# Kernel tuning notes

Hardware: AMD Instinct MI355X
Metric: run time of the kernel (lower is better)

Reference implementation:

```python
import jax, jax.numpy as jnp
import numpy as np
import math

B, L, C = 4096, 64, 256   # L == window_size
H = 8                     # num_heads
META_H = 384


def _rel_coords_log(W):
    # coords = meshgrid(arange(1), arange(W)) -> (2, W); first row is zeros
    c0 = jnp.zeros((W,), jnp.float32)
    c1 = jnp.arange(W, dtype=jnp.float32)
    coords = jnp.stack([c0, c1], axis=0)                      # (2, W)
    rel = coords[:, :, None] - coords[:, None, :]             # (2, W, W)
    rel = rel.transpose(1, 2, 0).reshape(-1, 2)               # (W*W, 2)
    return jnp.sign(rel) * jnp.log1p(jnp.abs(rel))


def setup_inputs() -> dict:
    key = jax.random.key(0)
    ks = jax.random.split(key, 8)
    s = 0.02
    return {
        "x": jax.random.normal(ks[0], (B, L, C), jnp.float32),
        "qkv_w": jax.random.normal(ks[1], (3 * C, C), jnp.float32) * s,
        "qkv_b": jnp.zeros((3 * C,), jnp.float32),
        "proj_w": jax.random.normal(ks[2], (C, C), jnp.float32) * s,
        "proj_b": jnp.zeros((C,), jnp.float32),
        "logit_scale": jnp.full((H,), math.log(10.0), jnp.float32),
        "mlp1_w": jax.random.normal(ks[3], (META_H, 2), jnp.float32) * s,
        "mlp1_b": jnp.zeros((META_H,), jnp.float32),
        "mlp2_w": jax.random.normal(ks[4], (H, META_H), jnp.float32) * s,
        "mlp2_b": jnp.zeros((H,), jnp.float32),
    }


def reference(x, qkv_w, qkv_b, proj_w, proj_b, logit_scale, mlp1_w, mlp1_b, mlp2_w, mlp2_b):
    b, l, c = x.shape
    h = H
    d = c // h
    qkv = x @ qkv_w.T + qkv_b                                 # (B, L, 3C)
    qkv = qkv.reshape(b, l, 3, h, d).transpose(2, 0, 3, 1, 4) # (3, B, H, L, D)
    q, k, v = qkv[0], qkv[1], qkv[2]
    # cosine attention: L2-normalize q, k (F.normalize, eps=1e-12)
    qn = q / jnp.maximum(jnp.linalg.norm(q, axis=-1, keepdims=True), 1e-12)
    kn = k / jnp.maximum(jnp.linalg.norm(k, axis=-1, keepdims=True), 1e-12)
    attn = jnp.einsum("bhld,bhmd->bhlm", qn, kn)              # (B, H, L, L)
    scale = jnp.exp(jnp.minimum(logit_scale, math.log(1.0 / 0.01)))
    attn = attn * scale.reshape(1, h, 1, 1)
    # MLP relative position bias
    rel = _rel_coords_log(l)                                  # (L*L, 2)
    hid = jax.nn.relu(rel @ mlp1_w.T + mlp1_b)                # (L*L, META_H)
    bias = (hid @ mlp2_w.T + mlp2_b).T.reshape(h, l, l)       # (H, L, L)
    attn = jax.nn.softmax(attn + bias[None], axis=-1)
    out = jnp.einsum("bhlm,bhmd->bhld", attn, v)              # (B, H, L, D)
    out = out.transpose(0, 2, 1, 3).reshape(b, l, c)
    return out @ proj_w.T + proj_b
```

## Files before the change

### kernel.cpp

```cpp
#include <hip/hip_runtime.h>
#include <hip/hip_bf16.h>

typedef __attribute__((ext_vector_type(4))) float f32x4;
typedef __attribute__((ext_vector_type(8))) short short8;
typedef __attribute__((ext_vector_type(4))) short short4_t;

#define NWIN 4096
#define LTOK 64
#define CDIM 256

static __device__ __forceinline__ short f2bf(float f) {
    __hip_bfloat16 h = __float2bfloat16(f);
    union { __hip_bfloat16 b; short s; } u; u.b = h;
    return u.s;
}

__global__ void prep_weights(const float* __restrict__ qw, const float* __restrict__ pw,
                             short* __restrict__ wqs, short* __restrict__ wps) {
    int i = blockIdx.x * 256 + threadIdx.x;
    if (i < 768 * 256) {
        int row = i >> 8, col = i & 255;
        int nt = row >> 4, lcr = row & 15;
        int kt = col >> 5, lg = (col >> 3) & 3, j = col & 7;
        wqs[(size_t)(((nt * 8 + kt) * 64) + lg * 16 + lcr) * 8 + j] = f2bf(qw[i]);
    }
    if (i < 256 * 256) {
        int row = i >> 8, col = i & 255;
        int ww = row >> 6, ntl = (row >> 4) & 3, lcr = row & 15;
        int h = col >> 5, lg = (col >> 3) & 3, j = col & 7;
        wps[(size_t)((((ww * 4 + ntl) * 8 + h) * 64) + lg * 16 + lcr) * 8 + j] = f2bf(pw[i]);
    }
}

__global__ void prep_bias(const float* __restrict__ w1, const float* __restrict__ b1,
                          const float* __restrict__ w2, const float* __restrict__ b2,
                          const float* __restrict__ lsc, float* __restrict__ biasT,
                          float* __restrict__ scT) {
    int t = threadIdx.x;
    if (t < 8) scT[t] = expf(fminf(lsc[t], logf(100.0f)));
    if (t < 127) {
        float delta = (float)(t - 63);
        float sg = (delta > 0.f) ? 1.f : ((delta < 0.f) ? -1.f : 0.f);
        float r = sg * log1pf(fabsf(delta));
        float acc[8];
        #pragma unroll
        for (int q = 0; q < 8; ++q) acc[q] = b2[q];
        for (int m = 0; m < 384; ++m) {
            float hid = fmaxf(fmaf(r, w1[m * 2 + 1], b1[m]), 0.f);
            #pragma unroll
            for (int q = 0; q < 8; ++q) acc[q] = fmaf(hid, w2[q * 384 + m], acc[q]);
        }
        #pragma unroll
        for (int q = 0; q < 8; ++q) biasT[q * 127 + t] = acc[q];
    }
}


__global__ void __launch_bounds__(256, 2)
fused_win_attn(const float* __restrict__ x,
               const float* __restrict__ qkv_b,
               const float* __restrict__ proj_b,
               const short* __restrict__ wqs,
               const short* __restrict__ wps,
               const float* __restrict__ biasT,
               const float* __restrict__ scT,
               float* __restrict__ out)
{
    __shared__ short XS[64 * 264];
    __shared__ short QG[64 * 72];
    __shared__ short KG[64 * 72];
    __shared__ short VT[64 * 72];
    __shared__ short PB[64 * 72];
    __shared__ short AO[64 * 40];
    __shared__ float NSQ[2 * 64 * 4];

    const int tid = threadIdx.x;
    const int w  = tid >> 6;
    const int l  = tid & 63;
    const int lg = l >> 4;
    const int lc = l & 15;
    const int blk = blockIdx.x;

    {
        const float* xb = x + (size_t)blk * (LTOK * CDIM);
        #pragma unroll
        for (int u = 0; u < 8; ++u) {
            int base = u * 2048 + tid * 8;
            f32x4 a = *(const f32x4*)(xb + base);
            f32x4 b = *(const f32x4*)(xb + base + 4);
            int r = base >> 8;
            int c = base & 255;
            short8 t;
            t[0] = f2bf(a[0]); t[1] = f2bf(a[1]); t[2] = f2bf(a[2]); t[3] = f2bf(a[3]);
            t[4] = f2bf(b[0]); t[5] = f2bf(b[1]); t[6] = f2bf(b[2]); t[7] = f2bf(b[3]);
            *(short8*)(XS + r * 264 + c) = t;
        }
    }

    f32x4 accP[4][4];
    #pragma unroll
    for (int a = 0; a < 4; ++a)
        #pragma unroll
        for (int bb = 0; bb < 4; ++bb)
            accP[a][bb] = (f32x4){0.f, 0.f, 0.f, 0.f};

    const f32x4 fzero = {0.f, 0.f, 0.f, 0.f};
    __syncthreads();

    #pragma unroll 1
    for (int g = 0; g < 4; ++g) {
        #pragma unroll
        for (int s = 0; s < 3; ++s) {
            const int cbt = s * 16 + g * 4 + w;
            const float bq = qkv_b[s * 256 + g * 64 + w * 16 + lc];
            f32x4 acc[4];
            acc[0] = acc[1] = acc[2] = acc[3] = fzero;
            #pragma unroll
            for (int kt = 0; kt < 8; ++kt) {
                short8 Bf = *(const short8*)(wqs + (size_t)((cbt * 8 + kt) * 64 + l) * 8);
                #pragma unroll
                for (int mt = 0; mt < 4; ++mt) {
                    short8 Af = *(const short8*)(XS + (mt * 16 + lc) * 264 + kt * 32 + lg * 8);
                    acc[mt] = __builtin_amdgcn_mfma_f32_16x16x32_bf16(Af, Bf, acc[mt], 0, 0, 0);
                }
            }
            if (s < 2) {
                short* dst = (s == 0) ? QG : KG;
                #pragma unroll
                for (int mt = 0; mt < 4; ++mt) {
                    #pragma unroll
                    for (int i = 0; i < 4; ++i) {
                        float v = acc[mt][i] + bq;
                        dst[(mt * 16 + lg * 4 + i) * 72 + (w * 16 + lc)] = f2bf(v);
                        float t = v * v;
                        t += __shfl_xor(t, 1);
                        t += __shfl_xor(t, 2);
                        t += __shfl_xor(t, 4);
                        t += __shfl_xor(t, 8);
                        if (lc == 0) NSQ[s * 256 + (mt * 16 + lg * 4 + i) * 4 + w] = t;
                    }
                }
            } else {
                #pragma unroll
                for (int mt = 0; mt < 4; ++mt) {
                    short4_t pk;
                    #pragma unroll
                    for (int i = 0; i < 4; ++i) pk[i] = f2bf(acc[mt][i] + bq);
                    *(short4_t*)(VT + (w * 16 + lc) * 72 + mt * 16 + lg * 4) = pk;
                }
            }
        }
        __syncthreads();

        #pragma unroll 1
        for (int hh = 0; hh < 2; ++hh) {
            const int h = 2 * g + hh;
            const float sc = scT[h];
            short8 Aq = *(const short8*)(QG + (w * 16 + lc) * 72 + hh * 32 + lg * 8);
            f32x4 pacc[4];
            #pragma unroll
            for (int nt = 0; nt < 4; ++nt) {
                short8 Bk = *(const short8*)(KG + (nt * 16 + lc) * 72 + hh * 32 + lg * 8);
                pacc[nt] = __builtin_amdgcn_mfma_f32_16x16x32_bf16(Aq, Bk, fzero, 0, 0, 0);
            }
            float invq[4], invk[4];
            #pragma unroll
            for (int i = 0; i < 4; ++i) {
                int r = w * 16 + lg * 4 + i;
                invq[i] = rsqrtf(NSQ[r * 4 + 2 * hh] + NSQ[r * 4 + 2 * hh + 1] + 1e-24f) * sc;
            }
            #pragma unroll
            for (int nt = 0; nt < 4; ++nt) {
                int rk = nt * 16 + lc;
                invk[nt] = rsqrtf(NSQ[256 + rk * 4 + 2 * hh] + NSQ[256 + rk * 4 + 2 * hh + 1] + 1e-24f);
            }
            float p[4][4];
            #pragma unroll
            for (int i = 0; i < 4; ++i) {
                int r = w * 16 + lg * 4 + i;
                #pragma unroll
                for (int nt = 0; nt < 4; ++nt) {
                    int c = nt * 16 + lc;
                    p[i][nt] = pacc[nt][i] * invq[i] * invk[nt] + biasT[h * 127 + r - c + 63];
                }
            }
            #pragma unroll
            for (int i = 0; i < 4; ++i) {
                float m = fmaxf(fmaxf(p[i][0], p[i][1]), fmaxf(p[i][2], p[i][3]));
                m = fmaxf(m, __shfl_xor(m, 1));
                m = fmaxf(m, __shfl_xor(m, 2));
                m = fmaxf(m, __shfl_xor(m, 4));
                m = fmaxf(m, __shfl_xor(m, 8));
                float ssum = 0.f;
                #pragma unroll
                for (int nt = 0; nt < 4; ++nt) { p[i][nt] = __expf(p[i][nt] - m); ssum += p[i][nt]; }
                ssum += __shfl_xor(ssum, 1);
                ssum += __shfl_xor(ssum, 2);
                ssum += __shfl_xor(ssum, 4);
                ssum += __shfl_xor(ssum, 8);
                float rinv = 1.f / ssum;
                #pragma unroll
                for (int nt = 0; nt < 4; ++nt)
                    PB[(w * 16 + lg * 4 + i) * 72 + nt * 16 + lc] = f2bf(p[i][nt] * rinv);
            }
            __syncthreads();

            f32x4 oacc[2];
            oacc[0] = oacc[1] = fzero;
            #pragma unroll
            for (int kt = 0; kt < 2; ++kt) {
                short8 Ap = *(const short8*)(PB + (w * 16 + lc) * 72 + kt * 32 + lg * 8);
                #pragma unroll
                for (int nt2 = 0; nt2 < 2; ++nt2) {
                    short8 Bv = *(const short8*)(VT + (hh * 32 + nt2 * 16 + lc) * 72 + kt * 32 + lg * 8);
                    oacc[nt2] = __builtin_amdgcn_mfma_f32_16x16x32_bf16(Ap, Bv, oacc[nt2], 0, 0, 0);
                }
            }
            #pragma unroll
            for (int nt2 = 0; nt2 < 2; ++nt2)
                #pragma unroll
                for (int i = 0; i < 4; ++i)
                    AO[(w * 16 + lg * 4 + i) * 40 + nt2 * 16 + lc] = f2bf(oacc[nt2][i]);
            __syncthreads();

            #pragma unroll
            for (int mt = 0; mt < 4; ++mt) {
                short8 Aa = *(const short8*)(AO + (mt * 16 + lc) * 40 + lg * 8);
                #pragma unroll
                for (int ntl = 0; ntl < 4; ++ntl) {
                    short8 Bp = *(const short8*)(wps + (size_t)(((w * 4 + ntl) * 8 + h) * 64 + l) * 8);
                    accP[mt][ntl] = __builtin_amdgcn_mfma_f32_16x16x32_bf16(Aa, Bp, accP[mt][ntl], 0, 0, 0);
                }
            }
        }
    }

    {
        float* ob = out + (size_t)blk * (LTOK * CDIM);
        float pbv[4];
        #pragma unroll
        for (int ntl = 0; ntl < 4; ++ntl) pbv[ntl] = proj_b[w * 64 + ntl * 16 + lc];
        #pragma unroll
        for (int mt = 0; mt < 4; ++mt)
            #pragma unroll
            for (int ntl = 0; ntl < 4; ++ntl)
                #pragma unroll
                for (int i = 0; i < 4; ++i)
                    ob[(mt * 16 + lg * 4 + i) * 256 + w * 64 + ntl * 16 + lc] = accP[mt][ntl][i] + pbv[ntl];
    }
}

extern "C" void kernel_launch(void* const* d_in, const int* in_sizes, int n_in,
                              void* d_out, int out_size, void* d_ws, size_t ws_size,
                              hipStream_t stream) {
    const float* x     = (const float*)d_in[0];
    const float* qkvw  = (const float*)d_in[1];
    const float* qkvb  = (const float*)d_in[2];
    const float* projw = (const float*)d_in[3];
    const float* projb = (const float*)d_in[4];
    const float* lsc   = (const float*)d_in[5];
    const float* w1    = (const float*)d_in[6];
    const float* b1    = (const float*)d_in[7];
    const float* w2    = (const float*)d_in[8];
    const float* b2    = (const float*)d_in[9];
    float* out = (float*)d_out;

    short* wqs   = (short*)d_ws;
    short* wps   = (short*)((char*)d_ws + 393216);
    float* biasT = (float*)((char*)d_ws + 524288);
    float* scT   = (float*)((char*)d_ws + 528384);

    const int nwin = in_sizes[0] / (LTOK * CDIM);

    prep_weights<<<768, 256, 0, stream>>>(qkvw, projw, wqs, wps);
    prep_bias<<<1, 128, 0, stream>>>(w1, b1, w2, b2, lsc, biasT, scT);
    fused_win_attn<<<nwin, 256, 0, stream>>>(x, qkvb, projb, wqs, wps, biasT, scT, out);
}
```

Before: 583.8 us.

## Use 512-thread blocks with per-head wave split and streamed x staging

Doubles the block to 8 waves. The QKV projection is split so each wave computes 3 column strips over 2 row tiles, and the two heads of a group run concurrently on wave halves with double PB/AO buffers. The full bf16 copy of x in LDS is replaced by a small fragment-layout buffer refilled from global memory in two K-halves on every head group, so x is re-read from global four times. This shrinks LDS use and raises per-CU wave count, at the cost of extra global traffic and more barriers.

```diff
diff --git a/kernel.cpp b/kernel.cpp
--- a/kernel.cpp
+++ b/kernel.cpp
@@ -5,7 +5,6 @@
 typedef __attribute__((ext_vector_type(8))) short short8;
 typedef __attribute__((ext_vector_type(4))) short short4_t;
 
-#define NWIN 4096
 #define LTOK 64
 #define CDIM 256
 
@@ -26,9 +25,9 @@
     }
     if (i < 256 * 256) {
         int row = i >> 8, col = i & 255;
-        int ww = row >> 6, ntl = (row >> 4) & 3, lcr = row & 15;
+        int gs = row >> 4, lcr = row & 15;
         int h = col >> 5, lg = (col >> 3) & 3, j = col & 7;
-        wps[(size_t)((((ww * 4 + ntl) * 8 + h) * 64) + lg * 16 + lcr) * 8 + j] = f2bf(pw[i]);
+        wps[(size_t)(((gs * 8 + h) * 64) + lg * 16 + lcr) * 8 + j] = f2bf(pw[i]);
     }
 }
 
@@ -56,7 +55,7 @@
 }
 
 
-__global__ void __launch_bounds__(256, 2)
+__global__ void __launch_bounds__(512, 4)
 fused_win_attn(const float* __restrict__ x,
                const float* __restrict__ qkv_b,
                const float* __restrict__ proj_b,
@@ -66,13 +65,13 @@
                const float* __restrict__ scT,
                float* __restrict__ out)
 {
-    __shared__ short XS[64 * 264];
+    __shared__ short XSF[16 * 64 * 8];
     __shared__ short QG[64 * 72];
     __shared__ short KG[64 * 72];
     __shared__ short VT[64 * 72];
-    __shared__ short PB[64 * 72];
-    __shared__ short AO[64 * 40];
-    __shared__ float NSQ[2 * 64 * 4];
+    __shared__ short PBs[2][64 * 72];
+    __shared__ short AOs[2][64 * 40];
+    __shared__ float NSQ[512];
 
     const int tid = threadIdx.x;
     const int w  = tid >> 6;
@@ -81,82 +80,98 @@
     const int lc = l & 15;
     const int blk = blockIdx.x;
 
-    {
-        const float* xb = x + (size_t)blk * (LTOK * CDIM);
-        #pragma unroll
-        for (int u = 0; u < 8; ++u) {
-            int base = u * 2048 + tid * 8;
-            f32x4 a = *(const f32x4*)(xb + base);
-            f32x4 b = *(const f32x4*)(xb + base + 4);
-            int r = base >> 8;
-            int c = base & 255;
-            short8 t;
-            t[0] = f2bf(a[0]); t[1] = f2bf(a[1]); t[2] = f2bf(a[2]); t[3] = f2bf(a[3]);
-            t[4] = f2bf(b[0]); t[5] = f2bf(b[1]); t[6] = f2bf(b[2]); t[7] = f2bf(b[3]);
-            *(short8*)(XS + r * 264 + c) = t;
-        }
-    }
-
-    f32x4 accP[4][4];
+    const float* xb = x + (size_t)blk * (LTOK * CDIM);
+
+    const int sb  = (w & 3) * 3;
+    const int mtb = (w >> 2) * 2;
+    const int hh  = w >> 2;
+    const int mw  = w & 3;
+
+    const int mtA = w & 3,        kA = w >> 2;
+    const int mtB = (8 + w) & 3,  kB = (8 + w) >> 2;
+    const float* gA = xb + (size_t)(mtA * 16 + lc) * CDIM + lg * 8;
+    const float* gB = xb + (size_t)(mtB * 16 + lc) * CDIM + lg * 8;
+    short* sA = XSF + (size_t)(w * 64 + l) * 8;
+    short* sB = XSF + (size_t)((8 + w) * 64 + l) * 8;
+
+    f32x4 accP[4][2];
     #pragma unroll
-    for (int a = 0; a < 4; ++a)
-        #pragma unroll
-        for (int bb = 0; bb < 4; ++bb)
-            accP[a][bb] = (f32x4){0.f, 0.f, 0.f, 0.f};
-
+    for (int a = 0; a < 4; ++a) { accP[a][0] = (f32x4){0,0,0,0}; accP[a][1] = (f32x4){0,0,0,0}; }
     const f32x4 fzero = {0.f, 0.f, 0.f, 0.f};
-    __syncthreads();
 
     #pragma unroll 1
     for (int g = 0; g < 4; ++g) {
-        #pragma unroll
-        for (int s = 0; s < 3; ++s) {
-            const int cbt = s * 16 + g * 4 + w;
-            const float bq = qkv_b[s * 256 + g * 64 + w * 16 + lc];
-            f32x4 acc[4];
-            acc[0] = acc[1] = acc[2] = acc[3] = fzero;
-            #pragma unroll
-            for (int kt = 0; kt < 8; ++kt) {
-                short8 Bf = *(const short8*)(wqs + (size_t)((cbt * 8 + kt) * 64 + l) * 8);
-                #pragma unroll
-                for (int mt = 0; mt < 4; ++mt) {
-                    short8 Af = *(const short8*)(XS + (mt * 16 + lc) * 264 + kt * 32 + lg * 8);
-                    acc[mt] = __builtin_amdgcn_mfma_f32_16x16x32_bf16(Af, Bf, acc[mt], 0, 0, 0);
-                }
-            }
-            if (s < 2) {
-                short* dst = (s == 0) ? QG : KG;
-                #pragma unroll
-                for (int mt = 0; mt < 4; ++mt) {
+        f32x4 acc[3][2];
+        #pragma unroll
+        for (int t = 0; t < 3; ++t) { acc[t][0] = fzero; acc[t][1] = fzero; }
+
+        #pragma unroll 1
+        for (int ht = 0; ht < 2; ++ht) {
+            {
+                f32x4 a0 = *(const f32x4*)(gA + (ht * 4 + kA) * 32);
+                f32x4 a1 = *(const f32x4*)(gA + (ht * 4 + kA) * 32 + 4);
+                f32x4 b0 = *(const f32x4*)(gB + (ht * 4 + kB) * 32);
+                f32x4 b1 = *(const f32x4*)(gB + (ht * 4 + kB) * 32 + 4);
+                short8 ta, tb;
+                ta[0]=f2bf(a0[0]); ta[1]=f2bf(a0[1]); ta[2]=f2bf(a0[2]); ta[3]=f2bf(a0[3]);
+                ta[4]=f2bf(a1[0]); ta[5]=f2bf(a1[1]); ta[6]=f2bf(a1[2]); ta[7]=f2bf(a1[3]);
+                tb[0]=f2bf(b0[0]); tb[1]=f2bf(b0[1]); tb[2]=f2bf(b0[2]); tb[3]=f2bf(b0[3]);
+                tb[4]=f2bf(b1[0]); tb[5]=f2bf(b1[1]); tb[6]=f2bf(b1[2]); tb[7]=f2bf(b1[3]);
+                *(short8*)sA = ta;
+                *(short8*)sB = tb;
+            }
+            __syncthreads();
+            #pragma unroll
+            for (int ktL = 0; ktL < 4; ++ktL) {
+                short8 Af0 = *(const short8*)(XSF + (size_t)((ktL * 4 + mtb) * 64 + l) * 8);
+                short8 Af1 = *(const short8*)(XSF + (size_t)((ktL * 4 + mtb + 1) * 64 + l) * 8);
+                #pragma unroll
+                for (int tt = 0; tt < 3; ++tt) {
+                    const int strip = sb + tt;
+                    const int gnt = (strip >> 2) * 16 + g * 4 + (strip & 3);
+                    short8 Bf = *(const short8*)(wqs + (size_t)((gnt * 8 + ht * 4 + ktL) * 64 + l) * 8);
+                    acc[tt][0] = __builtin_amdgcn_mfma_f32_16x16x32_bf16(Af0, Bf, acc[tt][0], 0, 0, 0);
+                    acc[tt][1] = __builtin_amdgcn_mfma_f32_16x16x32_bf16(Af1, Bf, acc[tt][1], 0, 0, 0);
+                }
+            }
+            __syncthreads();
+        }
+
+        #pragma unroll
+        for (int tt = 0; tt < 3; ++tt) {
+            const int strip = sb + tt;
+            const int s = strip >> 2, nt = strip & 3;
+            const float bq = qkv_b[s * 256 + g * 64 + nt * 16 + lc];
+            #pragma unroll
+            for (int m = 0; m < 2; ++m) {
+                const int mt = mtb + m;
+                if (s == 2) {
+                    short4_t pk;
+                    #pragma unroll
+                    for (int i = 0; i < 4; ++i) pk[i] = f2bf(acc[tt][m][i] + bq);
+                    *(short4_t*)(VT + (nt * 16 + lc) * 72 + mt * 16 + lg * 4) = pk;
+                } else {
+                    short* dst = s ? KG : QG;
                     #pragma unroll
                     for (int i = 0; i < 4; ++i) {
-                        float v = acc[mt][i] + bq;
-                        dst[(mt * 16 + lg * 4 + i) * 72 + (w * 16 + lc)] = f2bf(v);
-                        float t = v * v;
-                        t += __shfl_xor(t, 1);
-                        t += __shfl_xor(t, 2);
-                        t += __shfl_xor(t, 4);
-                        t += __shfl_xor(t, 8);
-                        if (lc == 0) NSQ[s * 256 + (mt * 16 + lg * 4 + i) * 4 + w] = t;
+                        float v = acc[tt][m][i] + bq;
+                        dst[(mt * 16 + lg * 4 + i) * 72 + nt * 16 + lc] = f2bf(v);
+                        float t2 = v * v;
+                        t2 += __shfl_xor(t2, 1);
+                        t2 += __shfl_xor(t2, 2);
+                        t2 += __shfl_xor(t2, 4);
+                        t2 += __shfl_xor(t2, 8);
+                        if (lc == 0) NSQ[s * 256 + (mt * 16 + lg * 4 + i) * 4 + nt] = t2;
                     }
                 }
-            } else {
-                #pragma unroll
-                for (int mt = 0; mt < 4; ++mt) {
-                    short4_t pk;
-                    #pragma unroll
-                    for (int i = 0; i < 4; ++i) pk[i] = f2bf(acc[mt][i] + bq);
-                    *(short4_t*)(VT + (w * 16 + lc) * 72 + mt * 16 + lg * 4) = pk;
-                }
             }
         }
         __syncthreads();
 
-        #pragma unroll 1
-        for (int hh = 0; hh < 2; ++hh) {
+        {
             const int h = 2 * g + hh;
             const float sc = scT[h];
-            short8 Aq = *(const short8*)(QG + (w * 16 + lc) * 72 + hh * 32 + lg * 8);
+            short8 Aq = *(const short8*)(QG + (mw * 16 + lc) * 72 + hh * 32 + lg * 8);
             f32x4 pacc[4];
             #pragma unroll
             for (int nt = 0; nt < 4; ++nt) {
@@ -166,7 +181,7 @@
             float invq[4], invk[4];
             #pragma unroll
             for (int i = 0; i < 4; ++i) {
-                int r = w * 16 + lg * 4 + i;
+                int r = mw * 16 + lg * 4 + i;
                 invq[i] = rsqrtf(NSQ[r * 4 + 2 * hh] + NSQ[r * 4 + 2 * hh + 1] + 1e-24f) * sc;
             }
             #pragma unroll
@@ -177,7 +192,7 @@
             float p[4][4];
             #pragma unroll
             for (int i = 0; i < 4; ++i) {
-                int r = w * 16 + lg * 4 + i;
+                int r = mw * 16 + lg * 4 + i;
                 #pragma unroll
                 for (int nt = 0; nt < 4; ++nt) {
                     int c = nt * 16 + lc;
@@ -201,15 +216,17 @@
                 float rinv = 1.f / ssum;
                 #pragma unroll
                 for (int nt = 0; nt < 4; ++nt)
-                    PB[(w * 16 + lg * 4 + i) * 72 + nt * 16 + lc] = f2bf(p[i][nt] * rinv);
-            }
-            __syncthreads();
-
+                    PBs[hh][(mw * 16 + lg * 4 + i) * 72 + nt * 16 + lc] = f2bf(p[i][nt] * rinv);
+            }
+        }
+        __syncthreads();
+
+        {
             f32x4 oacc[2];
-            oacc[0] = oacc[1] = fzero;
+            oacc[0] = fzero; oacc[1] = fzero;
             #pragma unroll
             for (int kt = 0; kt < 2; ++kt) {
-                short8 Ap = *(const short8*)(PB + (w * 16 + lc) * 72 + kt * 32 + lg * 8);
+                short8 Ap = *(const short8*)(PBs[hh] + (mw * 16 + lc) * 72 + kt * 32 + lg * 8);
                 #pragma unroll
                 for (int nt2 = 0; nt2 < 2; ++nt2) {
                     short8 Bv = *(const short8*)(VT + (hh * 32 + nt2 * 16 + lc) * 72 + kt * 32 + lg * 8);
@@ -220,33 +237,35 @@
             for (int nt2 = 0; nt2 < 2; ++nt2)
                 #pragma unroll
                 for (int i = 0; i < 4; ++i)
-                    AO[(w * 16 + lg * 4 + i) * 40 + nt2 * 16 + lc] = f2bf(oacc[nt2][i]);
-            __syncthreads();
-
+                    AOs[hh][(mw * 16 + lg * 4 + i) * 40 + nt2 * 16 + lc] = f2bf(oacc[nt2][i]);
+        }
+        __syncthreads();
+
+        #pragma unroll
+        for (int hh2 = 0; hh2 < 2; ++hh2) {
+            const int h2 = 2 * g + hh2;
+            short8 Bp0 = *(const short8*)(wps + (size_t)((((w * 2 + 0) * 8 + h2) * 64) + l) * 8);
+            short8 Bp1 = *(const short8*)(wps + (size_t)((((w * 2 + 1) * 8 + h2) * 64) + l) * 8);
             #pragma unroll
             for (int mt = 0; mt < 4; ++mt) {
-                short8 Aa = *(const short8*)(AO + (mt * 16 + lc) * 40 + lg * 8);
-                #pragma unroll
-                for (int ntl = 0; ntl < 4; ++ntl) {
-                    short8 Bp = *(const short8*)(wps + (size_t)(((w * 4 + ntl) * 8 + h) * 64 + l) * 8);
-                    accP[mt][ntl] = __builtin_amdgcn_mfma_f32_16x16x32_bf16(Aa, Bp, accP[mt][ntl], 0, 0, 0);
-                }
+                short8 Aa = *(const short8*)(AOs[hh2] + (mt * 16 + lc) * 40 + lg * 8);
+                accP[mt][0] = __builtin_amdgcn_mfma_f32_16x16x32_bf16(Aa, Bp0, accP[mt][0], 0, 0, 0);
+                accP[mt][1] = __builtin_amdgcn_mfma_f32_16x16x32_bf16(Aa, Bp1, accP[mt][1], 0, 0, 0);
             }
         }
     }
 
     {
         float* ob = out + (size_t)blk * (LTOK * CDIM);
-        float pbv[4];
-        #pragma unroll
-        for (int ntl = 0; ntl < 4; ++ntl) pbv[ntl] = proj_b[w * 64 + ntl * 16 + lc];
+        float pb0 = proj_b[w * 32 + lc];
+        float pb1 = proj_b[w * 32 + 16 + lc];
         #pragma unroll
         for (int mt = 0; mt < 4; ++mt)
             #pragma unroll
-            for (int ntl = 0; ntl < 4; ++ntl)
-                #pragma unroll
-                for (int i = 0; i < 4; ++i)
-                    ob[(mt * 16 + lg * 4 + i) * 256 + w * 64 + ntl * 16 + lc] = accP[mt][ntl][i] + pbv[ntl];
+            for (int i = 0; i < 4; ++i) {
+                ob[(size_t)(mt * 16 + lg * 4 + i) * 256 + w * 32 + lc]      = accP[mt][0][i] + pb0;
+                ob[(size_t)(mt * 16 + lg * 4 + i) * 256 + w * 32 + 16 + lc] = accP[mt][1][i] + pb1;
+            }
     }
 }
 
@@ -274,5 +293,5 @@
 
     prep_weights<<<768, 256, 0, stream>>>(qkvw, projw, wqs, wps);
     prep_bias<<<1, 128, 0, stream>>>(w1, b1, w2, b2, lsc, biasT, scT);
-    fused_win_attn<<<nwin, 256, 0, stream>>>(x, qkvb, projb, wqs, wps, biasT, scT, out);
-}
+    fused_win_attn<<<nwin, 512, 0, stream>>>(x, qkvb, projb, wqs, wps, biasT, scT, out);
+}
```

Result: slower. 786.2 us (+34.7%).

## Keep X in registers, fragment-layout LDS, per-wave P buffer, batched projection

Applied to the files above, without the earlier changes.

Each wave now owns 16 token rows and holds its bf16 X fragments in registers, so the X staging area in LDS and its barrier are gone. Q, K, V, P and attention outputs are stored in a padded MFMA-fragment LDS layout. Each wave keeps its own softmax buffer, which drops the per-head barriers, and q norms are reduced in registers. The output projection runs once per head pair after a single barrier, and the smaller LDS footprint allows three blocks per CU. The risks are higher register pressure from the X fragments and the larger accumulator, which could cause spills under the tighter launch bound.

```diff
diff --git a/kernel.cpp b/kernel.cpp
--- a/kernel.cpp
+++ b/kernel.cpp
@@ -5,15 +5,16 @@
 typedef __attribute__((ext_vector_type(8))) short short8;
 typedef __attribute__((ext_vector_type(4))) short short4_t;
 
-#define NWIN 4096
 #define LTOK 64
 #define CDIM 256
+#define FRS 576
 
 static __device__ __forceinline__ short f2bf(float f) {
     __hip_bfloat16 h = __float2bfloat16(f);
     union { __hip_bfloat16 b; short s; } u; u.b = h;
     return u.s;
 }
+static __device__ __forceinline__ int KL(int l) { return l + (l >> 3); }
 
 __global__ void prep_weights(const float* __restrict__ qw, const float* __restrict__ pw,
                              short* __restrict__ wqs, short* __restrict__ wps) {
@@ -26,9 +27,9 @@
     }
     if (i < 256 * 256) {
         int row = i >> 8, col = i & 255;
-        int ww = row >> 6, ntl = (row >> 4) & 3, lcr = row & 15;
+        int gs = row >> 4, lcr = row & 15;
         int h = col >> 5, lg = (col >> 3) & 3, j = col & 7;
-        wps[(size_t)((((ww * 4 + ntl) * 8 + h) * 64) + lg * 16 + lcr) * 8 + j] = f2bf(pw[i]);
+        wps[(size_t)(((gs * 8 + h) * 64) + lg * 16 + lcr) * 8 + j] = f2bf(pw[i]);
     }
 }
 
@@ -56,7 +57,7 @@
 }
 
 
-__global__ void __launch_bounds__(256, 2)
+__global__ void __launch_bounds__(256, 3)
 fused_win_attn(const float* __restrict__ x,
                const float* __restrict__ qkv_b,
                const float* __restrict__ proj_b,
@@ -66,34 +67,35 @@
                const float* __restrict__ scT,
                float* __restrict__ out)
 {
-    __shared__ short XS[64 * 264];
-    __shared__ short QG[64 * 72];
-    __shared__ short KG[64 * 72];
-    __shared__ short VT[64 * 72];
-    __shared__ short PB[64 * 72];
-    __shared__ short AO[64 * 40];
-    __shared__ float NSQ[2 * 64 * 4];
+    __shared__ short SH[23040];
+    __shared__ float NSQK[128];
 
     const int tid = threadIdx.x;
     const int w  = tid >> 6;
     const int l  = tid & 63;
     const int lg = l >> 4;
     const int lc = l & 15;
+    const int li4 = lg * 4;
     const int blk = blockIdx.x;
-
+    const int klb = KL(l) * 8;
+
+    short* QGF = SH;
+    short* KGF = SH + 4608;
+    short* VTF = SH + 9216;
+    short* AOF = SH + 13824;
+    short* PW  = SH + 18432 + w * (2 * FRS);
+
+    short8 xf[8];
     {
-        const float* xb = x + (size_t)blk * (LTOK * CDIM);
-        #pragma unroll
-        for (int u = 0; u < 8; ++u) {
-            int base = u * 2048 + tid * 8;
-            f32x4 a = *(const f32x4*)(xb + base);
-            f32x4 b = *(const f32x4*)(xb + base + 4);
-            int r = base >> 8;
-            int c = base & 255;
+        const float* xr = x + (size_t)blk * (LTOK * CDIM) + (size_t)(w * 16 + lc) * CDIM + lg * 8;
+        #pragma unroll
+        for (int kt = 0; kt < 8; ++kt) {
+            f32x4 a = *(const f32x4*)(xr + kt * 32);
+            f32x4 b = *(const f32x4*)(xr + kt * 32 + 4);
             short8 t;
-            t[0] = f2bf(a[0]); t[1] = f2bf(a[1]); t[2] = f2bf(a[2]); t[3] = f2bf(a[3]);
-            t[4] = f2bf(b[0]); t[5] = f2bf(b[1]); t[6] = f2bf(b[2]); t[7] = f2bf(b[3]);
-            *(short8*)(XS + r * 264 + c) = t;
+            t[0]=f2bf(a[0]); t[1]=f2bf(a[1]); t[2]=f2bf(a[2]); t[3]=f2bf(a[3]);
+            t[4]=f2bf(b[0]); t[5]=f2bf(b[1]); t[6]=f2bf(b[2]); t[7]=f2bf(b[3]);
+            xf[kt] = t;
         }
     }
 
@@ -101,88 +103,97 @@
     #pragma unroll
     for (int a = 0; a < 4; ++a)
         #pragma unroll
-        for (int bb = 0; bb < 4; ++bb)
-            accP[a][bb] = (f32x4){0.f, 0.f, 0.f, 0.f};
-
+        for (int b = 0; b < 4; ++b) accP[a][b] = (f32x4){0,0,0,0};
     const f32x4 fzero = {0.f, 0.f, 0.f, 0.f};
-    __syncthreads();
 
     #pragma unroll 1
     for (int g = 0; g < 4; ++g) {
-        #pragma unroll
-        for (int s = 0; s < 3; ++s) {
-            const int cbt = s * 16 + g * 4 + w;
-            const float bq = qkv_b[s * 256 + g * 64 + w * 16 + lc];
-            f32x4 acc[4];
-            acc[0] = acc[1] = acc[2] = acc[3] = fzero;
+        float rnq[2][4], rnk[2][4];
+        #pragma unroll
+        for (int hh = 0; hh < 2; ++hh)
+            #pragma unroll
+            for (int i = 0; i < 4; ++i) { rnq[hh][i] = 1e-24f; rnk[hh][i] = 1e-24f; }
+
+        #pragma unroll
+        for (int sg = 0; sg < 6; ++sg) {
+            const int st0 = sg * 2, st1 = sg * 2 + 1;
+            const int gnt0 = (st0 >> 2) * 16 + g * 4 + (st0 & 3);
+            const int gnt1 = (st1 >> 2) * 16 + g * 4 + (st1 & 3);
+            const short* wb0 = wqs + ((size_t)(gnt0 * 8) * 64 + l) * 8;
+            const short* wb1 = wqs + ((size_t)(gnt1 * 8) * 64 + l) * 8;
+            f32x4 a0 = fzero, a1 = fzero;
             #pragma unroll
             for (int kt = 0; kt < 8; ++kt) {
-                short8 Bf = *(const short8*)(wqs + (size_t)((cbt * 8 + kt) * 64 + l) * 8);
-                #pragma unroll
-                for (int mt = 0; mt < 4; ++mt) {
-                    short8 Af = *(const short8*)(XS + (mt * 16 + lc) * 264 + kt * 32 + lg * 8);
-                    acc[mt] = __builtin_amdgcn_mfma_f32_16x16x32_bf16(Af, Bf, acc[mt], 0, 0, 0);
-                }
-            }
-            if (s < 2) {
-                short* dst = (s == 0) ? QG : KG;
-                #pragma unroll
-                for (int mt = 0; mt < 4; ++mt) {
+                short8 Bf0 = *(const short8*)(wb0 + kt * 512);
+                short8 Bf1 = *(const short8*)(wb1 + kt * 512);
+                a0 = __builtin_amdgcn_mfma_f32_16x16x32_bf16(xf[kt], Bf0, a0, 0, 0, 0);
+                a1 = __builtin_amdgcn_mfma_f32_16x16x32_bf16(xf[kt], Bf1, a1, 0, 0, 0);
+            }
+            #pragma unroll
+            for (int e = 0; e < 2; ++e) {
+                const int strip = e ? st1 : st0;
+                const f32x4 av = e ? a1 : a0;
+                const int s = strip >> 2, nt = strip & 3;
+                const float bq = qkv_b[s * 256 + g * 64 + nt * 16 + lc];
+                if (s < 2) {
+                    short* base = (s ? KGF : QGF) + ((nt >> 1) * 4 + w) * FRS;
+                    const int lgc = (nt & 1) * 2 + (lc >> 3);
                     #pragma unroll
                     for (int i = 0; i < 4; ++i) {
-                        float v = acc[mt][i] + bq;
-                        dst[(mt * 16 + lg * 4 + i) * 72 + (w * 16 + lc)] = f2bf(v);
-                        float t = v * v;
-                        t += __shfl_xor(t, 1);
-                        t += __shfl_xor(t, 2);
-                        t += __shfl_xor(t, 4);
-                        t += __shfl_xor(t, 8);
-                        if (lc == 0) NSQ[s * 256 + (mt * 16 + lg * 4 + i) * 4 + w] = t;
+                        float v = av[i] + bq;
+                        if (s == 0) rnq[nt >> 1][i] = fmaf(v, v, rnq[nt >> 1][i]);
+                        else        rnk[nt >> 1][i] = fmaf(v, v, rnk[nt >> 1][i]);
+                        const int l2 = lgc * 16 + li4 + i;
+                        base[KL(l2) * 8 + (lc & 7)] = f2bf(v);
                     }
-                }
-            } else {
-                #pragma unroll
-                for (int mt = 0; mt < 4; ++mt) {
+                } else {
+                    short* base = VTF + ((w >> 1) * 4 + nt) * FRS;
+                    const int l2 = ((w & 1) * 2 + (lg >> 1)) * 16 + lc;
                     short4_t pk;
                     #pragma unroll
-                    for (int i = 0; i < 4; ++i) pk[i] = f2bf(acc[mt][i] + bq);
-                    *(short4_t*)(VT + (w * 16 + lc) * 72 + mt * 16 + lg * 4) = pk;
+                    for (int i = 0; i < 4; ++i) pk[i] = f2bf(av[i] + bq);
+                    *(short4_t*)(base + KL(l2) * 8 + (li4 & 7)) = pk;
                 }
             }
         }
+        float invqb[2][4];
+        #pragma unroll
+        for (int hh = 0; hh < 2; ++hh)
+            #pragma unroll
+            for (int i = 0; i < 4; ++i) {
+                float t = rnq[hh][i];
+                t += __shfl_xor(t, 1); t += __shfl_xor(t, 2);
+                t += __shfl_xor(t, 4); t += __shfl_xor(t, 8);
+                invqb[hh][i] = rsqrtf(t);
+                float u = rnk[hh][i];
+                u += __shfl_xor(u, 1); u += __shfl_xor(u, 2);
+                u += __shfl_xor(u, 4); u += __shfl_xor(u, 8);
+                if (lc == 0) NSQK[hh * 64 + w * 16 + li4 + i] = u;
+            }
         __syncthreads();
 
         #pragma unroll 1
         for (int hh = 0; hh < 2; ++hh) {
             const int h = 2 * g + hh;
             const float sc = scT[h];
-            short8 Aq = *(const short8*)(QG + (w * 16 + lc) * 72 + hh * 32 + lg * 8);
+            short8 Aq = *(const short8*)(QGF + (hh * 4 + w) * FRS + klb);
             f32x4 pacc[4];
             #pragma unroll
             for (int nt = 0; nt < 4; ++nt) {
-                short8 Bk = *(const short8*)(KG + (nt * 16 + lc) * 72 + hh * 32 + lg * 8);
+                short8 Bk = *(const short8*)(KGF + (hh * 4 + nt) * FRS + klb);
                 pacc[nt] = __builtin_amdgcn_mfma_f32_16x16x32_bf16(Aq, Bk, fzero, 0, 0, 0);
             }
-            float invq[4], invk[4];
+            float invk[4];
+            #pragma unroll
+            for (int nt = 0; nt < 4; ++nt) invk[nt] = rsqrtf(NSQK[hh * 64 + nt * 16 + lc]);
+            const float* bt = biasT + h * 127 + w * 16 + 63 - lc;
+            float p[4][4];
             #pragma unroll
             for (int i = 0; i < 4; ++i) {
-                int r = w * 16 + lg * 4 + i;
-                invq[i] = rsqrtf(NSQ[r * 4 + 2 * hh] + NSQ[r * 4 + 2 * hh + 1] + 1e-24f) * sc;
-            }
-            #pragma unroll
-            for (int nt = 0; nt < 4; ++nt) {
-                int rk = nt * 16 + lc;
-                invk[nt] = rsqrtf(NSQ[256 + rk * 4 + 2 * hh] + NSQ[256 + rk * 4 + 2 * hh + 1] + 1e-24f);
-            }
-            float p[4][4];
-            #pragma unroll
-            for (int i = 0; i < 4; ++i) {
-                int r = w * 16 + lg * 4 + i;
-                #pragma unroll
-                for (int nt = 0; nt < 4; ++nt) {
-                    int c = nt * 16 + lc;
-                    p[i][nt] = pacc[nt][i] * invq[i] * invk[nt] + biasT[h * 127 + r - c + 63];
-                }
+                const float iq = invqb[hh][i] * sc;
+                #pragma unroll
+                for (int nt = 0; nt < 4; ++nt)
+                    p[i][nt] = pacc[nt][i] * iq * invk[nt] + bt[li4 + i - nt * 16];
             }
             #pragma unroll
             for (int i = 0; i < 4; ++i) {
@@ -198,55 +209,67 @@
                 ssum += __shfl_xor(ssum, 2);
                 ssum += __shfl_xor(ssum, 4);
                 ssum += __shfl_xor(ssum, 8);
-                float rinv = 1.f / ssum;
-                #pragma unroll
-                for (int nt = 0; nt < 4; ++nt)
-                    PB[(w * 16 + lg * 4 + i) * 72 + nt * 16 + lc] = f2bf(p[i][nt] * rinv);
-            }
-            __syncthreads();
-
+                const float rinv = 1.f / ssum;
+                #pragma unroll
+                for (int nt = 0; nt < 4; ++nt) p[i][nt] *= rinv;
+            }
+            #pragma unroll
+            for (int i = 0; i < 4; ++i)
+                #pragma unroll
+                for (int nt = 0; nt < 4; ++nt) {
+                    const int l2 = ((nt & 1) * 2 + (lc >> 3)) * 16 + li4 + i;
+                    PW[(nt >> 1) * FRS + KL(l2) * 8 + (lc & 7)] = f2bf(p[i][nt]);
+                }
             f32x4 oacc[2];
-            oacc[0] = oacc[1] = fzero;
-            #pragma unroll
-            for (int kt = 0; kt < 2; ++kt) {
-                short8 Ap = *(const short8*)(PB + (w * 16 + lc) * 72 + kt * 32 + lg * 8);
-                #pragma unroll
-                for (int nt2 = 0; nt2 < 2; ++nt2) {
-                    short8 Bv = *(const short8*)(VT + (hh * 32 + nt2 * 16 + lc) * 72 + kt * 32 + lg * 8);
-                    oacc[nt2] = __builtin_amdgcn_mfma_f32_16x16x32_bf16(Ap, Bv, oacc[nt2], 0, 0, 0);
+            oacc[0] = fzero; oacc[1] = fzero;
+            #pragma unroll
+            for (int ktp = 0; ktp < 2; ++ktp) {
+                short8 Ap = *(const short8*)(PW + ktp * FRS + klb);
+                #pragma unroll
+                for (int ndv = 0; ndv < 2; ++ndv) {
+                    short8 Bv = *(const short8*)(VTF + (ktp * 4 + hh * 2 + ndv) * FRS + klb);
+                    oacc[ndv] = __builtin_amdgcn_mfma_f32_16x16x32_bf16(Ap, Bv, oacc[ndv], 0, 0, 0);
                 }
             }
             #pragma unroll
-            for (int nt2 = 0; nt2 < 2; ++nt2)
-                #pragma unroll
-                for (int i = 0; i < 4; ++i)
-                    AO[(w * 16 + lg * 4 + i) * 40 + nt2 * 16 + lc] = f2bf(oacc[nt2][i]);
-            __syncthreads();
-
-            #pragma unroll
-            for (int mt = 0; mt < 4; ++mt) {
-                short8 Aa = *(const short8*)(AO + (mt * 16 + lc) * 40 + lg * 8);
-                #pragma unroll
-                for (int ntl = 0; ntl < 4; ++ntl) {
-                    short8 Bp = *(const short8*)(wps + (size_t)(((w * 4 + ntl) * 8 + h) * 64 + l) * 8);
-                    accP[mt][ntl] = __builtin_amdgcn_mfma_f32_16x16x32_bf16(Aa, Bp, accP[mt][ntl], 0, 0, 0);
+            for (int ndv = 0; ndv < 2; ++ndv)
+                #pragma unroll
+                for (int i = 0; i < 4; ++i) {
+                    const int l2 = (ndv * 2 + (lc >> 3)) * 16 + li4 + i;
+                    AOF[(hh * 4 + w) * FRS + KL(l2) * 8 + (lc & 7)] = f2bf(oacc[ndv][i]);
                 }
+        }
+        __syncthreads();
+
+        #pragma unroll
+        for (int hh2 = 0; hh2 < 2; ++hh2) {
+            const int h2 = 2 * g + hh2;
+            short8 Aa0 = *(const short8*)(AOF + (hh2 * 4 + 0) * FRS + klb);
+            short8 Aa1 = *(const short8*)(AOF + (hh2 * 4 + 1) * FRS + klb);
+            short8 Aa2 = *(const short8*)(AOF + (hh2 * 4 + 2) * FRS + klb);
+            short8 Aa3 = *(const short8*)(AOF + (hh2 * 4 + 3) * FRS + klb);
+            #pragma unroll
+            for (int ntl = 0; ntl < 4; ++ntl) {
+                short8 Bp = *(const short8*)(wps + ((size_t)((w * 4 + ntl) * 8 + h2) * 64 + l) * 8);
+                accP[0][ntl] = __builtin_amdgcn_mfma_f32_16x16x32_bf16(Aa0, Bp, accP[0][ntl], 0, 0, 0);
+                accP[1][ntl] = __builtin_amdgcn_mfma_f32_16x16x32_bf16(Aa1, Bp, accP[1][ntl], 0, 0, 0);
+                accP[2][ntl] = __builtin_amdgcn_mfma_f32_16x16x32_bf16(Aa2, Bp, accP[2][ntl], 0, 0, 0);
+                accP[3][ntl] = __builtin_amdgcn_mfma_f32_16x16x32_bf16(Aa3, Bp, accP[3][ntl], 0, 0, 0);
             }
         }
     }
 
     {
         float* ob = out + (size_t)blk * (LTOK * CDIM);
-        float pbv[4];
-        #pragma unroll
-        for (int ntl = 0; ntl < 4; ++ntl) pbv[ntl] = proj_b[w * 64 + ntl * 16 + lc];
-        #pragma unroll
-        for (int mt = 0; mt < 4; ++mt)
-            #pragma unroll
-            for (int ntl = 0; ntl < 4; ++ntl)
+        #pragma unroll
+        for (int ntl = 0; ntl < 4; ++ntl) {
+            const float pb = proj_b[w * 64 + ntl * 16 + lc];
+            #pragma unroll
+            for (int mt = 0; mt < 4; ++mt)
                 #pragma unroll
                 for (int i = 0; i < 4; ++i)
-                    ob[(mt * 16 + lg * 4 + i) * 256 + w * 64 + ntl * 16 + lc] = accP[mt][ntl][i] + pbv[ntl];
+                    ob[(size_t)(mt * 16 + li4 + i) * 256 + w * 64 + ntl * 16 + lc] = accP[mt][ntl][i] + pb;
+        }
     }
 }
 
```

Measured after the change: 736.5 us. 1.26x slower.
